# Optimization experiments

Hardware: AMD Instinct MI355X
Metric: run time of the kernel (lower is better)

Reference implementation:

```python
import jax, jax.numpy as jnp
import numpy as np

CUTOFF, WIDTH, DIM, N_CONV = 5.0, 0.1, 64, 3
N_CENTERS = int(np.ceil(CUTOFF / WIDTH))            # 50
CENTERS = np.linspace(0.0, CUTOFF, N_CENTERS)       # RBF centers
GAP = float(CENTERS[1] - CENTERS[0])                # center spacing, coef = -1/GAP


def sp(x):
    # torch.nn.Softplus(beta=0.5, threshold=14): linear when 0.5*x > 14
    return jnp.where(x > 28.0, x, 2.0 * jax.nn.softplus(0.5 * x))


def setup_inputs() -> dict:
    key = jax.random.key(0)
    ks = jax.random.split(key, 32)
    N, E, K, NSEL, ESEL = 50000, 1600000, 20000, 5000, 20000
    f = jnp.float32
    nrm = lambda k, s, sc=0.1: jax.random.normal(k, s, dtype=f) * sc
    inp = {
        "emb": nrm(ks[0], (100, DIM), 1.0),
        "dist": jax.random.uniform(ks[1], (E,), f, 0.1, CUTOFF),
        "edge_mask": nrm(ks[2], (N_CENTERS,)),
        "conv_w1": nrm(ks[3], (N_CONV, DIM, DIM)),
        "cf_w1": nrm(ks[4], (N_CONV, DIM, N_CENTERS)),
        "cf_b1": nrm(ks[5], (N_CONV, DIM)),
        "cf_w2": nrm(ks[6], (N_CONV, DIM, DIM)),
        "cf_b2": nrm(ks[7], (N_CONV, DIM)),
        "nl2_w": nrm(ks[8], (N_CONV, DIM, DIM)),
        "nl2_b": nrm(ks[9], (N_CONV, DIM)),
        "nl3_w": nrm(ks[10], (N_CONV, DIM, DIM)),
        "nl3_b": nrm(ks[11], (N_CONV, DIM)),
        "nt1_w": nrm(ks[12], (32, DIM)),
        "nt1_b": nrm(ks[13], (32,)),
        "nt2_w": nrm(ks[14], (3, 32)),
        "nt2_b": nrm(ks[15], (3,)),
        "et1_w": nrm(ks[16], (64, 2 * DIM)),
        "et1_b": nrm(ks[17], (64,)),
        "et2_w": nrm(ks[18], (5, 64)),
        "et2_b": nrm(ks[19], (5,)),
        "node_type": jax.random.randint(ks[20], (N,), 0, 100),
        "src": jax.random.randint(ks[21], (E,), 0, N),
        "dst": jax.random.randint(ks[22], (E,), 0, N),
        "select_edge_index": jax.random.randint(ks[23], (K,), 0, E),
        "node_index": jax.random.randint(ks[24], (NSEL,), 0, N),
        "source_index": jax.random.randint(ks[25], (ESEL,), 0, N),
        "target_index": jax.random.randint(ks[26], (ESEL,), 0, N),
    }
    return inp


def reference(emb, dist, edge_mask, conv_w1, cf_w1, cf_b1, cf_w2, cf_b2,
              nl2_w, nl2_b, nl3_w, nl3_b, nt1_w, nt1_b, nt2_w, nt2_b,
              et1_w, et1_b, et2_w, et2_b,
              node_type, src, dst, select_edge_index, node_index,
              source_index, target_index):
    N = node_type.shape[0]
    centers = jnp.asarray(CENTERS, dtype=dist.dtype)
    # RBF edge features [E, 50]: exp(-(d - c)^2 / gap)
    rbf = jnp.exp((-1.0 / GAP) * (dist[:, None] - centers[None, :]) ** 2)
    # overwrite masked edges with learned edge_mask vector
    rbf = rbf.at[select_edge_index].set(edge_mask.astype(rbf.dtype))
    node = emb[node_type]                               # [N, 64]
    for i in range(N_CONV):                             # Interaction layers
        new_node = node @ conv_w1[i].T                  # bias-free projection
        h = sp(rbf @ cf_w1[i].T + cf_b1[i]) @ cf_w2[i].T + cf_b2[i]   # [E,64] filters
        msg = new_node[src] * h                         # u_mul_e
        agg = jax.ops.segment_sum(msg, dst, num_segments=N)          # sum reduce
        node = node + (sp(agg @ nl2_w[i].T + nl2_b[i]) @ nl3_w[i].T + nl3_b[i])
    ns = node[node_index]                               # [NSEL, 64]
    node_logits = (ns @ nt1_w.T + nt1_b) @ nt2_w.T + nt2_b           # [NSEL, 3]
    ef = jnp.concatenate([node[source_index], node[target_index]], axis=1)  # [ESEL,128]
    edge_logits = (ef @ et1_w.T + et1_b) @ et2_w.T + et2_b           # [ESEL, 5]
    return node_logits, edge_logits
```

## Files before the change

### kernel.cpp

```cpp
#include <hip/hip_runtime.h>
#include <hip/hip_bf16.h>

#define DIM 64
#define NC 50
#define TABN 4096
#define TABP (TABN + 2)
#define EPB 4096
#define NBMAX 512

typedef short bf16x8 __attribute__((ext_vector_type(8)));
typedef float f32x4  __attribute__((ext_vector_type(4)));
#define MFMA(a,b,c) __builtin_amdgcn_mfma_f32_16x16x32_bf16(a,b,c,0,0,0)

__device__ __forceinline__ float sp_f(float x){
  float e = __expf(0.5f*x);
  float s = 2.0f*__logf(1.0f+e);
  return x > 28.0f ? x : s;
}

__device__ __forceinline__ float rdl(float v, int l){
  return __int_as_float(__builtin_amdgcn_readlane(__float_as_int(v), l));
}

__device__ __forceinline__ unsigned short b16(float x){
  __hip_bfloat16 h = __float2bfloat16(x);
  return __builtin_bit_cast(unsigned short, h);
}

__device__ __forceinline__ void wsplit(float x, unsigned short& h, unsigned short& l){
  h = b16(x);
  float hf = __uint_as_float(((unsigned int)h) << 16);
  l = b16(x - hf);
}


__global__ __launch_bounds__(256) void bhist_kernel(const int* __restrict__ dst,
                                                    unsigned int* __restrict__ gbcnt,
                                                    unsigned int* __restrict__ flagbits,
                                                    int E, int NB, int FW){
  __shared__ unsigned int cnt[NBMAX];
  int tid = threadIdx.x;
  for (int b=tid; b<NB; b+=256) cnt[b] = 0;
  __syncthreads();
  int e0 = blockIdx.x*EPB, eend = min(e0+EPB, E);
  for (int e=e0+tid; e<eend; e+=256) atomicAdd(&cnt[dst[e]>>7], 1u);
  for (int w = blockIdx.x*256+tid; w < FW; w += gridDim.x*256) flagbits[w] = 0;
  __syncthreads();
  for (int b=tid; b<NB; b+=256) if (cnt[b]) atomicAdd(&gbcnt[b], cnt[b]);
}

__global__ void sel_mark_kernel(const int* __restrict__ sel,
                                unsigned int* __restrict__ flagbits, int K){
  int id = blockIdx.x*256 + threadIdx.x;
  if (id < K){ int e = sel[id]; atomicOr(&flagbits[e>>5], 1u << (e&31)); }
}

__global__ __launch_bounds__(NBMAX) void bscan_kernel(const unsigned int* __restrict__ gbcnt,
                                                      unsigned int* __restrict__ bscan,
                                                      unsigned int* __restrict__ gcursor,
                                                      int* __restrict__ offs,
                                                      int NB, int N, int E){
  __shared__ unsigned int s[NBMAX];
  int tid = threadIdx.x;
  unsigned int v = (tid < NB) ? gbcnt[tid] : 0;
  s[tid] = v;
  __syncthreads();
  for (int off=1; off<NBMAX; off<<=1){
    unsigned int u = (tid >= off) ? s[tid-off] : 0;
    __syncthreads();
    s[tid] += u;
    __syncthreads();
  }
  unsigned int excl = s[tid] - v;
  if (tid < NB){ bscan[tid] = excl; gcursor[tid] = excl; }
  if (tid == NB-1) bscan[NB] = excl + v;
  if (tid == 0) offs[N] = E;
}

__global__ __launch_bounds__(256) void passA_kernel(const int* __restrict__ dst,
                                                    const int* __restrict__ src,
                                                    const float* __restrict__ dist,
                                                    const unsigned int* __restrict__ flagbits,
                                                    unsigned int* __restrict__ gcursor,
                                                    unsigned long long* __restrict__ bbuf,
                                                    int E, int NB){
  __shared__ unsigned int cnt[NBMAX];
  __shared__ unsigned int base[NBMAX];
  int tid = threadIdx.x;
  for (int b=tid; b<NB; b+=256) cnt[b] = 0;
  __syncthreads();
  int e0 = blockIdx.x*EPB, eend = min(e0+EPB, E);
  for (int e=e0+tid; e<eend; e+=256) atomicAdd(&cnt[dst[e]>>7], 1u);
  __syncthreads();
  for (int b=tid; b<NB; b+=256){
    unsigned int c = cnt[b];
    base[b] = c ? atomicAdd(&gcursor[b], c) : 0u;
    cnt[b] = 0;
  }
  __syncthreads();
  for (int e=e0+tid; e<eend; e+=256){
    int d = dst[e];
    int b = d >> 7;
    unsigned int loc = atomicAdd(&cnt[b], 1u);
    float t = fminf(dist[e], 5.f) * ((float)TABN/5.0f);
    int idx = (int)(t + 0.5f); if (idx > TABN) idx = TABN;
    if ((flagbits[e>>5] >> (e&31)) & 1u) idx = TABN+1;
    unsigned int lo = ((unsigned int)src[e] << 16) | (unsigned int)idx;
    unsigned int hi = (unsigned int)(d & 127);
    bbuf[base[b] + loc] = ((unsigned long long)hi << 32) | lo;
  }
}

__global__ __launch_bounds__(256) void passB_kernel(const unsigned long long* __restrict__ bbuf,
                                                    const unsigned int* __restrict__ bscan,
                                                    int* __restrict__ offs,
                                                    unsigned int* __restrict__ csr,
                                                    int N){
  __shared__ unsigned int cnt[128];
  __shared__ unsigned int excl[128];
  int b = blockIdx.x, tid = threadIdx.x;
  unsigned int s0 = bscan[b];
  int m = (int)(bscan[b+1] - s0);
  if (tid < 128) cnt[tid] = 0;
  __syncthreads();
  for (int i=tid; i<m; i+=256)
    atomicAdd(&cnt[(unsigned int)(bbuf[s0+i] >> 32)], 1u);
  __syncthreads();
  if (tid < 128) excl[tid] = cnt[tid];
  __syncthreads();
  for (int off=1; off<128; off<<=1){
    unsigned int v = (tid < 128 && tid >= off) ? excl[tid-off] : 0;
    __syncthreads();
    if (tid < 128) excl[tid] += v;
    __syncthreads();
  }
  int node0 = b << 7;
  if (tid < 128){
    unsigned int ex = excl[tid] - cnt[tid];
    int n = node0 + tid;
    if (n < N) offs[n] = (int)(s0 + ex);
    excl[tid] = ex;
    cnt[tid] = 0;
  }
  __syncthreads();
  for (int i=tid; i<m; i+=256){
    unsigned long long v = bbuf[s0+i];
    unsigned int hi = (unsigned int)(v >> 32);
    unsigned int loc = atomicAdd(&cnt[hi], 1u);
    csr[s0 + excl[hi] + loc] = (unsigned int)v;
  }
}


__global__ void prep_transpose_kernel(const float* __restrict__ cf_w2,
                                      const float* __restrict__ et1_w,
                                      const float* __restrict__ nt1_w,
                                      const float* __restrict__ cf_w1,
                                      float* __restrict__ w2t,
                                      float* __restrict__ et1t,
                                      float* __restrict__ nt1t,
                                      float* __restrict__ w1t){
  int id = blockIdx.x*256 + threadIdx.x;
  if (id < 3*4096){
    int i = id >> 12, r = id & 4095;
    int k = r >> 6, j = r & 63;
    w2t[id]  = cf_w2[i*4096 + j*64 + k];
  }
  if (id < 128*64){
    int k = id >> 6, j = id & 63;
    et1t[id] = et1_w[j*128 + k];
  }
  if (id < 64*32){
    int k = id >> 5, j = id & 31;
    nt1t[id] = nt1_w[j*64 + k];
  }
  if (id < 3*NC*DIM){
    int l = id / (NC*DIM);
    int r = id - l*(NC*DIM);
    int m = r >> 6, k = r & 63;
    w1t[id] = cf_w1[l*DIM*NC + k*NC + m];
  }
}


__global__ __launch_bounds__(256) void table_kernel(const float* __restrict__ edge_mask,
                                                    const float* __restrict__ w1t,
                                                    const float* __restrict__ cf_b1,
                                                    const float* __restrict__ w2t,
                                                    const float* __restrict__ cf_b2,
                                                    __hip_bfloat16* __restrict__ tabb){
  int row = blockIdx.x*4 + (threadIdx.x >> 6);
  if (row >= 3*TABP) return;
  int l = row / TABP, p = row - l*TABP;
  int lane = threadIdx.x & 63;
  float rbfv = 0.f;
  if (lane < NC){
    if (p == TABN+1) rbfv = edge_mask[lane];
    else {
      float d = (float)p * (5.0f/(float)TABN);
      float c = (lane == NC-1) ? 5.0f : (float)((double)lane * (5.0/49.0));
      float df = d - c;
      rbfv = __expf((float)(-1.0/(5.0/49.0)) * df * df);
    }
  }
  const float* W1 = w1t + l*NC*DIM;
  float t = cf_b1[l*DIM + lane];
  #pragma unroll 10
  for (int m=0;m<NC;m++)
    t = fmaf(rdl(rbfv, m), W1[m*64 + lane], t);
  float su = sp_f(t);
  const float* W2 = w2t + l*DIM*DIM;
  float h = cf_b2[l*DIM + lane];
  #pragma unroll 16
  for (int k=0;k<DIM;k++)
    h = fmaf(rdl(su, k), W2[k*64 + lane], h);
  tabb[((size_t)l*TABP + p)*DIM + lane] = __float2bfloat16(h);
}


__device__ __forceinline__ void stage_w2(const float* __restrict__ src,
                                         char* hi, char* lo, int tid){
  #pragma unroll
  for (int ii=0; ii<8; ii++){
    int i = tid + ii*256;
    int row = i >> 5, cp = i & 31;
    float2 v = *(const float2*)(src + row*64 + cp*2);
    unsigned short hx,lx,hy,ly;
    wsplit(v.x, hx, lx);
    wsplit(v.y, hy, ly);
    int off = row*128 + ((cp*4) ^ ((row&7)<<4));
    *(unsigned int*)(hi + off) = (unsigned int)hx | ((unsigned int)hy << 16);
    *(unsigned int*)(lo + off) = (unsigned int)lx | ((unsigned int)ly << 16);
  }
}

__device__ __forceinline__ bf16x8 ldfrag(const char* base, int rowbase, int ks, int lane){
  int r = lane & 15;
  int off = (ks<<6) + ((lane>>4)<<4);
  return *(const bf16x8*)(base + (rowbase + r)*128 + (off ^ ((r & 7)<<4)));
}

__device__ __forceinline__ void stx(char* XH, char* XLo, int row, int col, float v){
  unsigned short h,l;
  wsplit(v, h, l);
  int off = row*128 + ((col*2) ^ ((row&7)<<4));
  *(unsigned short*)(XH + off) = h;
  *(unsigned short*)(XLo + off) = l;
}

#define MM6(XH_, XLo_, WH_, WLo_, NT, ACC) \
  { ACC = MFMA(ah0, ldfrag(WH_,  (NT)*16, 0, lane), ACC); \
    ACC = MFMA(ah1, ldfrag(WH_,  (NT)*16, 1, lane), ACC); \
    ACC = MFMA(ah0, ldfrag(WLo_, (NT)*16, 0, lane), ACC); \
    ACC = MFMA(ah1, ldfrag(WLo_, (NT)*16, 1, lane), ACC); \
    ACC = MFMA(al0, ldfrag(WH_,  (NT)*16, 0, lane), ACC); \
    ACC = MFMA(al1, ldfrag(WH_,  (NT)*16, 1, lane), ACC); }

#define LDA(XH_, XLo_) \
  bf16x8 ah0 = ldfrag(XH_, mb, 0, lane), ah1 = ldfrag(XH_, mb, 1, lane); \
  bf16x8 al0 = ldfrag(XLo_, mb, 0, lane), al1 = ldfrag(XLo_, mb, 1, lane);

__global__ __launch_bounds__(256) void node_init6_kernel(const float* __restrict__ emb,
                                                         const int* __restrict__ node_type,
                                                         const float* __restrict__ cw1_0,
                                                         float* __restrict__ node,
                                                         __hip_bfloat16* __restrict__ nnb, int N){
  __shared__ __align__(16) char WL[16384];
  __shared__ __align__(16) char XP[16384];
  char *WH = WL, *WLo = WL + 8192;
  char *XH = XP, *XLo = XP + 8192;
  int tid = threadIdx.x, lane = tid & 63, wv = tid >> 6;
  int nb = blockIdx.x*64, mb = wv*16;
  stage_w2(cw1_0, WH, WLo, tid);
  #pragma unroll
  for (int t=0;t<16;t++){
    int row = mb + t, n = nb + row;
    int ty = (n < N) ? node_type[n] : 0;
    float v = emb[(long)ty*64 + lane];
    if (n < N) node[(long)n*64 + lane] = v;
    stx(XH, XLo, row, lane, v);
  }
  __syncthreads();
  LDA(XH, XLo)
  #pragma unroll
  for (int nt=0; nt<4; nt++){
    f32x4 acc = {0.f,0.f,0.f,0.f};
    MM6(XH, XLo, WH, WLo, nt, acc)
    int col = nt*16 + (lane&15);
    #pragma unroll
    for (int v=0; v<4; v++){
      int n = nb + mb + ((lane>>4)<<2) + v;
      if (n < N) ((unsigned short*)nnb)[(long)n*64 + col] = b16(acc[v]);
    }
  }
}

template<bool PRODUCE_NN>
__global__ __launch_bounds__(256) void node_update6_kernel(float* __restrict__ node,
                                                           const float* __restrict__ agg,
                                                           const float* __restrict__ nl2_w,
                                                           const float* __restrict__ nl2_b,
                                                           const float* __restrict__ nl3_w,
                                                           const float* __restrict__ nl3_b,
                                                           const float* __restrict__ cw1_next,
                                                           __hip_bfloat16* __restrict__ nnb, int N){
  __shared__ __align__(16) char WL[49152];
  __shared__ __align__(16) char XP[16384];
  char *W2H = WL,          *W2L = WL + 8192;
  char *W3H = WL + 16384,  *W3L = WL + 24576;
  char *W1H = WL + 32768,  *W1L = WL + 40960;
  char *XH = XP, *XLo = XP + 8192;
  int tid = threadIdx.x, lane = tid & 63, wv = tid >> 6;
  int nb = blockIdx.x*64, mb = wv*16;
  stage_w2(nl2_w, W2H, W2L, tid);
  stage_w2(nl3_w, W3H, W3L, tid);
  if (PRODUCE_NN) stage_w2(cw1_next, W1H, W1L, tid);
  #pragma unroll
  for (int t=0;t<16;t++){
    int row = mb + t, n = nb + row;
    float v = (n < N) ? agg[(long)n*64 + lane] : 0.f;
    stx(XH, XLo, row, lane, v);
  }
  __syncthreads();
  {
    LDA(XH, XLo)
    #pragma unroll
    for (int nt=0; nt<4; nt++){
      float bb = nl2_b[nt*16 + (lane&15)];
      f32x4 acc = {bb,bb,bb,bb};
      MM6(XH, XLo, W2H, W2L, nt, acc)
      int col = nt*16 + (lane&15);
      #pragma unroll
      for (int v=0; v<4; v++){
        int row = mb + ((lane>>4)<<2) + v;
        stx(XH, XLo, row, col, sp_f(acc[v]));
      }
    }
  }
  {
    LDA(XH, XLo)
    #pragma unroll
    for (int nt=0; nt<4; nt++){
      float bb = nl3_b[nt*16 + (lane&15)];
      f32x4 acc = {bb,bb,bb,bb};
      MM6(XH, XLo, W3H, W3L, nt, acc)
      int col = nt*16 + (lane&15);
      #pragma unroll
      for (int v=0; v<4; v++){
        int row = mb + ((lane>>4)<<2) + v;
        int n = nb + row;
        float nv = 0.f;
        if (n < N){
          long g = (long)n*64 + col;
          nv = node[g] + acc[v];
          node[g] = nv;
        }
        stx(XH, XLo, row, col, nv);
      }
    }
  }
  if (PRODUCE_NN){
    LDA(XH, XLo)
    #pragma unroll
    for (int nt=0; nt<4; nt++){
      f32x4 acc = {0.f,0.f,0.f,0.f};
      MM6(XH, XLo, W1H, W1L, nt, acc)
      int col = nt*16 + (lane&15);
      #pragma unroll
      for (int v=0; v<4; v++){
        int n = nb + mb + ((lane>>4)<<2) + v;
        if (n < N) ((unsigned short*)nnb)[(long)n*64 + col] = b16(acc[v]);
      }
    }
  }
}

__global__ __launch_bounds__(256) void agg_kernel(const unsigned int* __restrict__ csr,
                                                  const int* __restrict__ offs,
                                                  const unsigned short* __restrict__ tab,
                                                  const unsigned short* __restrict__ nnb,
                                                  float* __restrict__ agg, int N){
  int n = blockIdx.x*4 + (threadIdx.x >> 6);
  int lane = threadIdx.x & 63;
  if (n >= N) return;
  int beg = offs[n], end = offs[n+1];
  float acc = 0.f;
  for (int c = beg; c < end; c += 64){
    int m = end - c; if (m > 64) m = 64;
    unsigned int pkv = csr[c + (lane < m ? lane : 0)];
    int q = 0;
    for (; q + 8 <= m; q += 8){
      #pragma unroll
      for (int u=0; u<8; u++){
        unsigned int p = (unsigned int)__builtin_amdgcn_readlane((int)pkv, q+u);
        int idx = p & 0xFFFF, s = p >> 16;
        float a  = __uint_as_float(((unsigned int)tab[idx*64 + lane]) << 16);
        float nn = __uint_as_float(((unsigned int)nnb[(long)s*64 + lane]) << 16);
        acc = fmaf(nn, a, acc);
      }
    }
    for (; q < m; q++){
      unsigned int p = (unsigned int)__builtin_amdgcn_readlane((int)pkv, q);
      int idx = p & 0xFFFF, s = p >> 16;
      float a  = __uint_as_float(((unsigned int)tab[idx*64 + lane]) << 16);
      float nn = __uint_as_float(((unsigned int)nnb[(long)s*64 + lane]) << 16);
      acc = fmaf(nn, a, acc);
    }
  }
  agg[(long)n*64 + lane] = acc;
}


__global__ __launch_bounds__(256) void node_head_kernel(const float* __restrict__ node,
                                                        const int* __restrict__ nidx,
                                                        const float* __restrict__ nt1t,
                                                        const float* __restrict__ nt1_b,
                                                        const float* __restrict__ nt2_w,
                                                        const float* __restrict__ nt2_b,
                                                        float* __restrict__ out, int NSEL){
  int r = __builtin_amdgcn_readfirstlane(blockIdx.x*4 + (threadIdx.x>>6));
  int lane = threadIdx.x & 63;
  if (r >= NSEL) return;
  long n = nidx[r];
  const float* x = node + n*64;
  float u = 0.f;
  if (lane < 32){
    u = nt1_b[lane];
    #pragma unroll
    for (int k=0;k<DIM;k++) u += x[k]*nt1t[k*32 + lane];
  }
  #pragma unroll
  for (int q=0;q<3;q++){
    float v = (lane < 32) ? u*nt2_w[q*32 + lane] : 0.f;
    #pragma unroll
    for (int o=32;o>=1;o>>=1) v += __shfl_xor(v, o);
    if (lane == 0) out[(long)r*3 + q] = nt2_b[q] + v;
  }
}

__global__ __launch_bounds__(256) void edge_head_kernel(const float* __restrict__ node,
                                                        const int* __restrict__ sidx,
                                                        const int* __restrict__ tidx,
                                                        const float* __restrict__ et1t,
                                                        const float* __restrict__ et1_b,
                                                        const float* __restrict__ et2_w,
                                                        const float* __restrict__ et2_b,
                                                        float* __restrict__ out, int ESEL){
  int wid = threadIdx.x >> 6, lane = threadIdx.x & 63;
  int r0 = (blockIdx.x*4 + wid)*4;
  if (r0 >= ESEL) return;
  float xs[4], xt[4], acc[4];
  #pragma unroll
  for (int i=0;i<4;i++){
    int r = r0+i < ESEL ? r0+i : ESEL-1;
    long s = sidx[r], t = tidx[r];
    xs[i] = node[s*64 + lane];
    xt[i] = node[t*64 + lane];
    acc[i] = et1_b[lane];
  }
  #pragma unroll 16
  for (int k=0;k<DIM;k++){
    float w1 = et1t[k*64 + lane];
    float w2 = et1t[(64+k)*64 + lane];
    #pragma unroll
    for (int i=0;i<4;i++){
      acc[i] = fmaf(rdl(xs[i], k), w1, acc[i]);
      acc[i] = fmaf(rdl(xt[i], k), w2, acc[i]);
    }
  }
  #pragma unroll
  for (int i=0;i<4;i++){
    if (r0+i >= ESEL) break;
    #pragma unroll
    for (int q=0;q<5;q++){
      float v = acc[i]*et2_w[q*64 + lane];
      #pragma unroll
      for (int o=32;o>=1;o>>=1) v += __shfl_xor(v, o);
      if (lane == 0) out[(long)(r0+i)*5 + q] = et2_b[q] + v;
    }
  }
}


extern "C" void kernel_launch(void* const* d_in, const int* in_sizes, int n_in,
                              void* d_out, int out_size, void* d_ws, size_t ws_size,
                              hipStream_t stream){
  const float* emb      = (const float*)d_in[0];
  const float* dist     = (const float*)d_in[1];
  const float* edge_mask= (const float*)d_in[2];
  const float* conv_w1  = (const float*)d_in[3];
  const float* cf_w1    = (const float*)d_in[4];
  const float* cf_b1    = (const float*)d_in[5];
  const float* cf_w2    = (const float*)d_in[6];
  const float* cf_b2    = (const float*)d_in[7];
  const float* nl2_w    = (const float*)d_in[8];
  const float* nl2_b    = (const float*)d_in[9];
  const float* nl3_w    = (const float*)d_in[10];
  const float* nl3_b    = (const float*)d_in[11];
  const float* nt1_w    = (const float*)d_in[12];
  const float* nt1_b    = (const float*)d_in[13];
  const float* nt2_w    = (const float*)d_in[14];
  const float* nt2_b    = (const float*)d_in[15];
  const float* et1_w    = (const float*)d_in[16];
  const float* et1_b    = (const float*)d_in[17];
  const float* et2_w    = (const float*)d_in[18];
  const float* et2_b    = (const float*)d_in[19];
  const int* node_type  = (const int*)d_in[20];
  const int* src        = (const int*)d_in[21];
  const int* dst        = (const int*)d_in[22];
  const int* sel        = (const int*)d_in[23];
  const int* node_index = (const int*)d_in[24];
  const int* source_index = (const int*)d_in[25];
  const int* target_index = (const int*)d_in[26];

  int E    = in_sizes[1];
  int N    = in_sizes[20];
  int K    = in_sizes[23];
  int NSEL = in_sizes[24];
  int ESEL = in_sizes[25];

  int NB  = (N + 127) >> 7;
  int FW  = (E + 31) >> 5;
  int nbE = (E + EPB - 1) / EPB;

  size_t N64 = (size_t)N*64;
  unsigned long long* bbuf = (unsigned long long*)d_ws;
  float* agg = (float*)d_ws;
  size_t aggsz = ((size_t)2*E > N64) ? (size_t)2*E : N64;
  float* p = (float*)d_ws + aggsz;
  float* node     = p; p += N64;
  __hip_bfloat16* nnb = (__hip_bfloat16*)p; p += N64/2;
  float* w2t      = p; p += 3*4096;
  float* et1t     = p; p += 128*64;
  float* nt1t     = p; p += 64*32;
  float* w1t      = p; p += 3*NC*DIM;
  __hip_bfloat16* tabb = (__hip_bfloat16*)p; p += (size_t)3*TABP*DIM/2;
  unsigned int* csr      = (unsigned int*)p; p += E;
  unsigned int* flagbits = (unsigned int*)p; p += FW;
  unsigned int* gbcnt    = (unsigned int*)p; p += NB;
  unsigned int* bscan    = (unsigned int*)p; p += NB+1;
  unsigned int* gcursor  = (unsigned int*)p; p += NB;
  int* offs              = (int*)p; p += N+1;

  hipMemsetAsync(gbcnt, 0, (size_t)NB*sizeof(int), stream);
  bhist_kernel<<<nbE, 256, 0, stream>>>(dst, gbcnt, flagbits, E, NB, FW);
  sel_mark_kernel<<<(K+255)/256, 256, 0, stream>>>(sel, flagbits, K);
  prep_transpose_kernel<<<48, 256, 0, stream>>>(cf_w2, et1_w, nt1_w, cf_w1,
                                                w2t, et1t, nt1t, w1t);
  bscan_kernel<<<1, NBMAX, 0, stream>>>(gbcnt, bscan, gcursor, offs, NB, N, E);
  passA_kernel<<<nbE, 256, 0, stream>>>(dst, src, dist, flagbits, gcursor, bbuf, E, NB);
  passB_kernel<<<NB, 256, 0, stream>>>(bbuf, bscan, offs, csr, N);
  table_kernel<<<(3*TABP+3)/4, 256, 0, stream>>>(edge_mask, w1t, cf_b1, w2t, cf_b2, tabb);

  int nbP  = (N+63)/64;
  int nb_agg = (N+3)/4;
  node_init6_kernel<<<nbP, 256, 0, stream>>>(emb, node_type, conv_w1, node, nnb, N);
  for (int l=0;l<3;l++){
    agg_kernel<<<nb_agg, 256, 0, stream>>>(csr, offs,
        (const unsigned short*)(tabb + (size_t)l*TABP*DIM),
        (const unsigned short*)nnb, agg, N);
    if (l < 2)
      node_update6_kernel<true><<<nbP, 256, 0, stream>>>(node, agg, nl2_w + l*4096, nl2_b + l*64,
          nl3_w + l*4096, nl3_b + l*64, conv_w1 + (l+1)*4096, nnb, N);
    else
      node_update6_kernel<false><<<nbP, 256, 0, stream>>>(node, agg, nl2_w + l*4096, nl2_b + l*64,
          nl3_w + l*4096, nl3_b + l*64, nullptr, nullptr, N);
  }

  node_head_kernel<<<(NSEL+3)/4, 256, 0, stream>>>(node, node_index,
      nt1t, nt1_b, nt2_w, nt2_b, (float*)d_out, NSEL);
  edge_head_kernel<<<(ESEL+15)/16, 256, 0, stream>>>(node, source_index, target_index,
      et1t, et1_b, et2_w, et2_b, (float*)d_out + (size_t)NSEL*3, ESEL);
}
```

Measured before the change: 337.3 us.

## Precompute bf16 hi/lo MFMA weight fragments once instead of per-block LDS staging

Adds a prep kernel that splits conv_w1, nl2 and nl3 weights into bf16 hi/lo parts and stores them in MFMA fragment order in global memory. The node init and update kernels then read B fragments directly from global/L2 instead of having every block stage and split weights into up to 48KB of shared memory. This removes redundant per-block conversion work and LDS use, which may raise occupancy, at the cost of more global loads per MFMA. Edges per block in the histogram/partition passes are also halved.

```diff
diff --git a/kernel.cpp b/kernel.cpp
--- a/kernel.cpp
+++ b/kernel.cpp
@@ -5,7 +5,7 @@
 #define NC 50
 #define TABN 4096
 #define TABP (TABN + 2)
-#define EPB 4096
+#define EPB 2048
 #define NBMAX 512
 
 typedef short bf16x8 __attribute__((ext_vector_type(8)));
@@ -180,6 +180,34 @@
     int m = r >> 6, k = r & 63;
     w1t[id] = cf_w1[l*DIM*NC + k*NC + m];
   }
+}
+
+
+__global__ void wprep2_kernel(const float* __restrict__ cw1,
+                              const float* __restrict__ nl2,
+                              const float* __restrict__ nl3,
+                              bf16x8* __restrict__ wfrag){
+  int id = blockIdx.x*256 + threadIdx.x;
+  if (id >= 9*8*64) return;
+  int lane = id & 63;
+  int f8 = (id >> 6) & 7;
+  int m  = id >> 9;
+  int nt = f8 >> 1, ks = f8 & 1;
+  const float* W = (m < 3) ? (cw1 + m*4096)
+                 : (m < 6) ? (nl2 + (m-3)*4096)
+                           : (nl3 + (m-6)*4096);
+  int j  = nt*16 + (lane & 15);
+  int k0 = ks*32 + (lane >> 4)*8;
+  bf16x8 vh, vl;
+  #pragma unroll
+  for (int u=0;u<8;u++){
+    unsigned short h,l;
+    wsplit(W[j*64 + k0 + u], h, l);
+    vh[u] = (short)h; vl[u] = (short)l;
+  }
+  int fb = m*16 + nt*4 + ks*2;
+  wfrag[(fb+0)*64 + lane] = vh;
+  wfrag[(fb+1)*64 + lane] = vl;
 }
 
 
@@ -218,22 +246,6 @@
 }
 
 
-__device__ __forceinline__ void stage_w2(const float* __restrict__ src,
-                                         char* hi, char* lo, int tid){
-  #pragma unroll
-  for (int ii=0; ii<8; ii++){
-    int i = tid + ii*256;
-    int row = i >> 5, cp = i & 31;
-    float2 v = *(const float2*)(src + row*64 + cp*2);
-    unsigned short hx,lx,hy,ly;
-    wsplit(v.x, hx, lx);
-    wsplit(v.y, hy, ly);
-    int off = row*128 + ((cp*4) ^ ((row&7)<<4));
-    *(unsigned int*)(hi + off) = (unsigned int)hx | ((unsigned int)hy << 16);
-    *(unsigned int*)(lo + off) = (unsigned int)lx | ((unsigned int)ly << 16);
-  }
-}
-
 __device__ __forceinline__ bf16x8 ldfrag(const char* base, int rowbase, int ks, int lane){
   int r = lane & 15;
   int off = (ks<<6) + ((lane>>4)<<4);
@@ -248,30 +260,27 @@
   *(unsigned short*)(XLo + off) = l;
 }
 
-#define MM6(XH_, XLo_, WH_, WLo_, NT, ACC) \
-  { ACC = MFMA(ah0, ldfrag(WH_,  (NT)*16, 0, lane), ACC); \
-    ACC = MFMA(ah1, ldfrag(WH_,  (NT)*16, 1, lane), ACC); \
-    ACC = MFMA(ah0, ldfrag(WLo_, (NT)*16, 0, lane), ACC); \
-    ACC = MFMA(ah1, ldfrag(WLo_, (NT)*16, 1, lane), ACC); \
-    ACC = MFMA(al0, ldfrag(WH_,  (NT)*16, 0, lane), ACC); \
-    ACC = MFMA(al1, ldfrag(WH_,  (NT)*16, 1, lane), ACC); }
+#define MM6G(WF, NT, ACC) \
+  { ACC = MFMA(ah0, (WF)[((NT)*4+0)*64 + lane], ACC); \
+    ACC = MFMA(ah1, (WF)[((NT)*4+2)*64 + lane], ACC); \
+    ACC = MFMA(ah0, (WF)[((NT)*4+1)*64 + lane], ACC); \
+    ACC = MFMA(ah1, (WF)[((NT)*4+3)*64 + lane], ACC); \
+    ACC = MFMA(al0, (WF)[((NT)*4+0)*64 + lane], ACC); \
+    ACC = MFMA(al1, (WF)[((NT)*4+2)*64 + lane], ACC); }
 
 #define LDA(XH_, XLo_) \
   bf16x8 ah0 = ldfrag(XH_, mb, 0, lane), ah1 = ldfrag(XH_, mb, 1, lane); \
   bf16x8 al0 = ldfrag(XLo_, mb, 0, lane), al1 = ldfrag(XLo_, mb, 1, lane);
 
-__global__ __launch_bounds__(256) void node_init6_kernel(const float* __restrict__ emb,
+__global__ __launch_bounds__(256) void node_init8_kernel(const float* __restrict__ emb,
                                                          const int* __restrict__ node_type,
-                                                         const float* __restrict__ cw1_0,
+                                                         const bf16x8* __restrict__ wf0,
                                                          float* __restrict__ node,
-                                                         __hip_bfloat16* __restrict__ nnb, int N){
-  __shared__ __align__(16) char WL[16384];
+                                                         unsigned short* __restrict__ nout, int N){
   __shared__ __align__(16) char XP[16384];
-  char *WH = WL, *WLo = WL + 8192;
   char *XH = XP, *XLo = XP + 8192;
   int tid = threadIdx.x, lane = tid & 63, wv = tid >> 6;
   int nb = blockIdx.x*64, mb = wv*16;
-  stage_w2(cw1_0, WH, WLo, tid);
   #pragma unroll
   for (int t=0;t<16;t++){
     int row = mb + t, n = nb + row;
@@ -285,36 +294,29 @@
   #pragma unroll
   for (int nt=0; nt<4; nt++){
     f32x4 acc = {0.f,0.f,0.f,0.f};
-    MM6(XH, XLo, WH, WLo, nt, acc)
+    MM6G(wf0, nt, acc)
     int col = nt*16 + (lane&15);
     #pragma unroll
     for (int v=0; v<4; v++){
       int n = nb + mb + ((lane>>4)<<2) + v;
-      if (n < N) ((unsigned short*)nnb)[(long)n*64 + col] = b16(acc[v]);
+      if (n < N) nout[(long)n*64 + col] = b16(acc[v]);
     }
   }
 }
 
 template<bool PRODUCE_NN>
-__global__ __launch_bounds__(256) void node_update6_kernel(float* __restrict__ node,
+__global__ __launch_bounds__(256) void node_update8_kernel(float* __restrict__ node,
                                                            const float* __restrict__ agg,
-                                                           const float* __restrict__ nl2_w,
+                                                           const bf16x8* __restrict__ wfA,
                                                            const float* __restrict__ nl2_b,
-                                                           const float* __restrict__ nl3_w,
+                                                           const bf16x8* __restrict__ wfB,
                                                            const float* __restrict__ nl3_b,
-                                                           const float* __restrict__ cw1_next,
-                                                           __hip_bfloat16* __restrict__ nnb, int N){
-  __shared__ __align__(16) char WL[49152];
+                                                           const bf16x8* __restrict__ wfC,
+                                                           unsigned short* __restrict__ nout, int N){
   __shared__ __align__(16) char XP[16384];
-  char *W2H = WL,          *W2L = WL + 8192;
-  char *W3H = WL + 16384,  *W3L = WL + 24576;
-  char *W1H = WL + 32768,  *W1L = WL + 40960;
   char *XH = XP, *XLo = XP + 8192;
   int tid = threadIdx.x, lane = tid & 63, wv = tid >> 6;
   int nb = blockIdx.x*64, mb = wv*16;
-  stage_w2(nl2_w, W2H, W2L, tid);
-  stage_w2(nl3_w, W3H, W3L, tid);
-  if (PRODUCE_NN) stage_w2(cw1_next, W1H, W1L, tid);
   #pragma unroll
   for (int t=0;t<16;t++){
     int row = mb + t, n = nb + row;
@@ -328,7 +330,7 @@
     for (int nt=0; nt<4; nt++){
       float bb = nl2_b[nt*16 + (lane&15)];
       f32x4 acc = {bb,bb,bb,bb};
-      MM6(XH, XLo, W2H, W2L, nt, acc)
+      MM6G(wfA, nt, acc)
       int col = nt*16 + (lane&15);
       #pragma unroll
       for (int v=0; v<4; v++){
@@ -343,7 +345,7 @@
     for (int nt=0; nt<4; nt++){
       float bb = nl3_b[nt*16 + (lane&15)];
       f32x4 acc = {bb,bb,bb,bb};
-      MM6(XH, XLo, W3H, W3L, nt, acc)
+      MM6G(wfB, nt, acc)
       int col = nt*16 + (lane&15);
       #pragma unroll
       for (int v=0; v<4; v++){
@@ -364,12 +366,12 @@
     #pragma unroll
     for (int nt=0; nt<4; nt++){
       f32x4 acc = {0.f,0.f,0.f,0.f};
-      MM6(XH, XLo, W1H, W1L, nt, acc)
+      MM6G(wfC, nt, acc)
       int col = nt*16 + (lane&15);
       #pragma unroll
       for (int v=0; v<4; v++){
         int n = nb + mb + ((lane>>4)<<2) + v;
-        if (n < N) ((unsigned short*)nnb)[(long)n*64 + col] = b16(acc[v]);
+        if (n < N) nout[(long)n*64 + col] = b16(acc[v]);
       }
     }
   }
@@ -529,11 +531,12 @@
   size_t aggsz = ((size_t)2*E > N64) ? (size_t)2*E : N64;
   float* p = (float*)d_ws + aggsz;
   float* node     = p; p += N64;
-  __hip_bfloat16* nnb = (__hip_bfloat16*)p; p += N64/2;
+  unsigned short* nnb = (unsigned short*)p; p += N64/2;
   float* w2t      = p; p += 3*4096;
   float* et1t     = p; p += 128*64;
   float* nt1t     = p; p += 64*32;
   float* w1t      = p; p += 3*NC*DIM;
+  bf16x8* wfrag   = (bf16x8*)p; p += 9*16*64*4;
   __hip_bfloat16* tabb = (__hip_bfloat16*)p; p += (size_t)3*TABP*DIM/2;
   unsigned int* csr      = (unsigned int*)p; p += E;
   unsigned int* flagbits = (unsigned int*)p; p += FW;
@@ -547,6 +550,7 @@
   sel_mark_kernel<<<(K+255)/256, 256, 0, stream>>>(sel, flagbits, K);
   prep_transpose_kernel<<<48, 256, 0, stream>>>(cf_w2, et1_w, nt1_w, cf_w1,
                                                 w2t, et1t, nt1t, w1t);
+  wprep2_kernel<<<18, 256, 0, stream>>>(conv_w1, nl2_w, nl3_w, wfrag);
   bscan_kernel<<<1, NBMAX, 0, stream>>>(gbcnt, bscan, gcursor, offs, NB, N, E);
   passA_kernel<<<nbE, 256, 0, stream>>>(dst, src, dist, flagbits, gcursor, bbuf, E, NB);
   passB_kernel<<<NB, 256, 0, stream>>>(bbuf, bscan, offs, csr, N);
@@ -554,17 +558,20 @@
 
   int nbP  = (N+63)/64;
   int nb_agg = (N+3)/4;
-  node_init6_kernel<<<nbP, 256, 0, stream>>>(emb, node_type, conv_w1, node, nnb, N);
+  node_init8_kernel<<<nbP, 256, 0, stream>>>(emb, node_type, wfrag, node, nnb, N);
   for (int l=0;l<3;l++){
     agg_kernel<<<nb_agg, 256, 0, stream>>>(csr, offs,
-        (const unsigned short*)(tabb + (size_t)l*TABP*DIM),
-        (const unsigned short*)nnb, agg, N);
+        (const unsigned short*)(tabb + (size_t)l*TABP*DIM), nnb, agg, N);
     if (l < 2)
-      node_update6_kernel<true><<<nbP, 256, 0, stream>>>(node, agg, nl2_w + l*4096, nl2_b + l*64,
-          nl3_w + l*4096, nl3_b + l*64, conv_w1 + (l+1)*4096, nnb, N);
+      node_update8_kernel<true><<<nbP, 256, 0, stream>>>(node, agg,
+          wfrag + (3+l)*16*64, nl2_b + l*64,
+          wfrag + (6+l)*16*64, nl3_b + l*64,
+          wfrag + (1+l)*16*64, nnb, N);
     else
-      node_update6_kernel<false><<<nbP, 256, 0, stream>>>(node, agg, nl2_w + l*4096, nl2_b + l*64,
-          nl3_w + l*4096, nl3_b + l*64, nullptr, nullptr, N);
+      node_update8_kernel<false><<<nbP, 256, 0, stream>>>(node, agg,
+          wfrag + (3+l)*16*64, nl2_b + l*64,
+          wfrag + (6+l)*16*64, nl3_b + l*64,
+          nullptr, nullptr, N);
   }
 
   node_head_kernel<<<(NSEL+3)/4, 256, 0, stream>>>(node, node_index,
```

Result: faster. 329.3 us (-2.3%).
